# Kernel tuning notes

Hardware: AMD Instinct MI355X
Metric: run time of the kernel (lower is better)

The kernel has to match this reference:

```python
import jax, jax.numpy as jnp
import numpy as np

B, T, D = 4, 2048, 1024
H, Dh = 16, 64
Q_LAT, KV_LAT, O_LAT = 512, 256, 512
ROPE = 32
FFN_RANK, FFN_INTER = 384, 4096
EPS = 1e-6
THETA = 10000.0


def rms_norm(x, w, eps=EPS):
    xf = x.astype(jnp.float32)
    var = jnp.mean(xf * xf, axis=-1, keepdims=True)
    return (w * (xf * jax.lax.rsqrt(var + eps))).astype(x.dtype)


def rotate_half(x):
    x1, x2 = jnp.split(x, 2, axis=-1)
    return jnp.concatenate([-x2, x1], axis=-1)


def setup_inputs() -> dict:
    key = jax.random.key(0)
    ks = jax.random.split(key, 12)
    s = lambda fan_in: 1.0 / np.sqrt(fan_in)
    inp = {
        "hidden_states": jax.random.normal(ks[0], (B, T, D), jnp.float32),
        "ln1_w": jnp.ones((D,), jnp.float32),
        "a_ln_w": jnp.ones((Q_LAT + KV_LAT,), jnp.float32),
        "qkv_a_w": jax.random.normal(ks[1], (D, Q_LAT + KV_LAT), jnp.float32) * s(D),
        "q_b_w": jax.random.normal(ks[2], (Q_LAT, H * Dh), jnp.float32) * s(Q_LAT),
        "kv_b_w": jax.random.normal(ks[3], (KV_LAT, 2 * H * Dh), jnp.float32) * s(KV_LAT),
        "o_a_w": jax.random.normal(ks[4], (H * Dh, O_LAT), jnp.float32) * s(H * Dh),
        "o_b_w": jax.random.normal(ks[5], (O_LAT, D), jnp.float32) * s(O_LAT),
        "ln2_w": jnp.ones((D,), jnp.float32),
        "ffn_in_a": jax.random.normal(ks[6], (D, FFN_RANK), jnp.float32) * s(D),
        "ffn_in_b": jax.random.normal(ks[7], (FFN_RANK, FFN_INTER), jnp.float32) * s(FFN_RANK),
        "ffn_out_a": jax.random.normal(ks[8], (FFN_INTER, FFN_RANK), jnp.float32) * s(FFN_INTER),
        "ffn_out_b": jax.random.normal(ks[9], (FFN_RANK, D), jnp.float32) * s(FFN_RANK),
    }
    # RoPE tables over first ROPE dims of each head
    inv_freq = 1.0 / (THETA ** (np.arange(0, ROPE, 2, dtype=np.float32) / ROPE))
    t = np.arange(T, dtype=np.float32)
    freqs = np.outer(t, inv_freq)                      # [T, ROPE/2]
    emb = np.concatenate([freqs, freqs], axis=-1)      # [T, ROPE]
    inp["cos"] = jnp.asarray(np.cos(emb), jnp.float32)
    inp["sin"] = jnp.asarray(np.sin(emb), jnp.float32)
    return inp


def reference(hidden_states, cos, sin, ln1_w, a_ln_w, qkv_a_w, q_b_w, kv_b_w,
              o_a_w, o_b_w, ln2_w, ffn_in_a, ffn_in_b, ffn_out_a, ffn_out_b):
    x = hidden_states
    # --- MLA attention (pre-norm) ---
    h = rms_norm(x, ln1_w)
    lat = rms_norm(h @ qkv_a_w, a_ln_w)                # [B,T,Q_LAT+KV_LAT]
    q_lat, kv_lat = jnp.split(lat, [Q_LAT], axis=-1)
    q = (q_lat @ q_b_w).reshape(B, T, H, Dh).transpose(0, 2, 1, 3)   # [B,H,T,Dh]
    kv = (kv_lat @ kv_b_w).reshape(B, T, H, 2 * Dh).transpose(0, 2, 1, 3)
    k, v = jnp.split(kv, 2, axis=-1)
    # partial RoPE on first ROPE dims
    c = cos[None, None]; s_ = sin[None, None]          # [1,1,T,ROPE]
    q_r, q_p = q[..., :ROPE], q[..., ROPE:]
    k_r, k_p = k[..., :ROPE], k[..., ROPE:]
    q = jnp.concatenate([q_r * c + rotate_half(q_r) * s_, q_p], axis=-1)
    k = jnp.concatenate([k_r * c + rotate_half(k_r) * s_, k_p], axis=-1)
    scores = jnp.einsum("bhqd,bhkd->bhqk", q, k) * (Dh ** -0.5)
    attn = jax.nn.softmax(scores, axis=-1)
    ctx = jnp.einsum("bhqk,bhkd->bhqd", attn, v)
    ctx = ctx.transpose(0, 2, 1, 3).reshape(B, T, H * Dh)
    attn_out = (ctx @ o_a_w) @ o_b_w                   # output subspace
    x = x + attn_out
    # --- decomposed FFN (pre-norm) ---
    h2 = rms_norm(x, ln2_w)
    ff = jax.nn.gelu((h2 @ ffn_in_a) @ ffn_in_b)
    ff = (ff @ ffn_out_a) @ ffn_out_b
    return x + ff
```

## Files before the change

### kernel.cpp

```cpp
#include <hip/hip_runtime.h>
#include <hip/hip_bf16.h>
#include <stdint.h>

#define NTOK 8192

typedef unsigned short u16;
typedef __attribute__((ext_vector_type(4))) float f32x4;
typedef __attribute__((ext_vector_type(8))) short s16x8;
typedef __attribute__((ext_vector_type(4))) short s16x4;
typedef __attribute__((ext_vector_type(8))) u16   u16x8;
typedef __attribute__((ext_vector_type(4))) u16   u16x4;

__device__ __forceinline__ float fast_exp2(float x) {
    return __builtin_amdgcn_exp2f(x);
}
__device__ __forceinline__ u16 f2bf(float f) {
    uint32_t u = __float_as_uint(f);
    u = (u + 0x7FFFu + ((u >> 16) & 1u)) >> 16;
    return (u16)u;
}
__device__ __forceinline__ u16 f2bf_fast(float f) {
    return (u16)((__float_as_uint(f) + 0x8000u) >> 16);
}
__device__ __forceinline__ float bf2f(u16 h) {
    return __uint_as_float(((uint32_t)h) << 16);
}
__device__ __forceinline__ void async_cp16(const void* g, void* l) {
    __builtin_amdgcn_global_load_lds(
        (const __attribute__((address_space(1))) void*)g,
        (__attribute__((address_space(3))) void*)l, 16, 0, 0);
}
__device__ __forceinline__ void wait_vm4()   { asm volatile("s_waitcnt vmcnt(4)" ::: "memory"); }
__device__ __forceinline__ void wait_vm0()   { asm volatile("s_waitcnt vmcnt(0)" ::: "memory"); }
__device__ __forceinline__ void wait_lgkm0() { asm volatile("s_waitcnt lgkmcnt(0)" ::: "memory"); }
__device__ __forceinline__ void raw_barrier(){ asm volatile("s_barrier" ::: "memory"); }

struct TDesc { const float* s; u16* d; int K; int N; int tile0; };
struct TPack { TDesc t[8]; };

__global__ __launch_bounds__(256) void k_transpose_all(TPack p)
{
    __shared__ float tile[32][33];
    int bid = blockIdx.x;
    int i = 0;
    #pragma unroll
    for (int j = 1; j < 8; j++) if (bid >= p.t[j].tile0) i = j;
    const float* src = p.t[i].s;
    u16* dst = p.t[i].d;
    int K = p.t[i].K, N = p.t[i].N;
    int local = bid - p.t[i].tile0;
    int nx = N >> 5;
    int n0 = (local % nx) * 32, k0 = (local / nx) * 32;
    int tx = threadIdx.x, ty = threadIdx.y;
    #pragma unroll
    for (int r = 0; r < 32; r += 8)
        tile[ty + r][tx] = src[(size_t)(k0 + ty + r) * N + n0 + tx];
    __syncthreads();
    #pragma unroll
    for (int r = 0; r < 32; r += 8)
        dst[(size_t)(n0 + ty + r) * K + k0 + tx] = f2bf(tile[tx][ty + r]);
}

__global__ __launch_bounds__(256) void k_cvt(
    const float* __restrict__ in, u16* __restrict__ out)
{
    int i = (blockIdx.x * 256 + threadIdx.x) * 4;
    f32x4 v = *(const f32x4*)&in[i];
    u16x4 o;
    #pragma unroll
    for (int j = 0; j < 4; j++) o[j] = f2bf(v[j]);
    *(u16x4*)&out[i] = o;
}

template<int W>
__global__ __launch_bounds__(256) void k_rmsnorm(
    const float* __restrict__ x, const float* __restrict__ w, u16* __restrict__ out)
{
    constexpr int E = W / 256;
    int row = blockIdx.x, tid = threadIdx.x;
    const float* xr = x + (size_t)row * W;
    float v[E]; float ss = 0.f;
    #pragma unroll
    for (int i = 0; i < E; i++) { v[i] = xr[tid + i * 256]; ss += v[i] * v[i]; }
    #pragma unroll
    for (int m = 1; m < 64; m <<= 1) ss += __shfl_xor(ss, m, 64);
    __shared__ float red[4];
    if ((tid & 63) == 0) red[tid >> 6] = ss;
    __syncthreads();
    ss = red[0] + red[1] + red[2] + red[3];
    float scale = rsqrtf(ss / (float)W + 1e-6f);
    u16* orow = out + (size_t)row * W;
    #pragma unroll
    for (int i = 0; i < E; i++)
        orow[tid + i * 256] = f2bf(w[tid + i * 256] * (v[i] * scale));
}

template<int EPI>
__global__ __launch_bounds__(256) void k_gemm(
    const u16* __restrict__ A, int lda,
    const u16* __restrict__ Bt, int ldb,
    int M, int N, int K,
    float* __restrict__ outF, u16* __restrict__ outB,
    const float* __restrict__ resid)
{
    __shared__ __align__(16) u16 As[2][4096];
    __shared__ __align__(16) u16 Bs[2][4096];
    int tid = threadIdx.x;
    int w = tid >> 6, lane = tid & 63;
    int m0 = blockIdx.y * 128, n0 = blockIdx.x * 128;
    int wm = w & 1, wn = w >> 1;
    int lr = lane & 15, lq = lane >> 4;

    f32x4 acc[4][4];
    #pragma unroll
    for (int i = 0; i < 4; i++)
        #pragma unroll
        for (int j = 0; j < 4; j++) acc[i][j] = (f32x4)(0.f);

    int ar = tid >> 2;
    int ac = (tid & 3) * 8;
    const u16* Ag = A  + (size_t)(m0 + ar) * lda + ac;
    const u16* Bg = Bt + (size_t)(n0 + ar) * ldb + ac;
    int lo = w * 512;

    auto stage = [&](int kt, int s) {
        const u16* a  = Ag + kt * 32;
        const u16* bp = Bg + kt * 32;
        async_cp16(a,                     &As[s][lo]);
        async_cp16(a + (size_t)64 * lda,  &As[s][lo + 2048]);
        async_cp16(bp,                    &Bs[s][lo]);
        async_cp16(bp + (size_t)64 * ldb, &Bs[s][lo + 2048]);
    };

    int nk = K >> 5;
    stage(0, 0);
    stage(1, 1);
    for (int k = 0; k < nk; k++) {
        if (k + 1 < nk) wait_vm4(); else wait_vm0();
        raw_barrier();
        int s = k & 1;
        s16x8 af[4], bfr[4];
        #pragma unroll
        for (int ms = 0; ms < 4; ms++)
            af[ms] = *reinterpret_cast<const s16x8*>(&As[s][(wm * 64 + ms * 16 + lr) * 32 + lq * 8]);
        #pragma unroll
        for (int ns = 0; ns < 4; ns++)
            bfr[ns] = *reinterpret_cast<const s16x8*>(&Bs[s][(wn * 64 + ns * 16 + lr) * 32 + lq * 8]);
        #pragma unroll
        for (int ms = 0; ms < 4; ms++)
            #pragma unroll
            for (int ns = 0; ns < 4; ns++)
                acc[ms][ns] = __builtin_amdgcn_mfma_f32_16x16x32_bf16(af[ms], bfr[ns], acc[ms][ns], 0, 0, 0);
        wait_lgkm0();
        raw_barrier();
        if (k + 2 < nk) stage(k + 2, s);
    }

    #pragma unroll
    for (int ms = 0; ms < 4; ms++) {
        #pragma unroll
        for (int ns = 0; ns < 4; ns++) {
            int col = n0 + wn * 64 + ns * 16 + lr;
            #pragma unroll
            for (int r = 0; r < 4; r++) {
                int row = m0 + wm * 64 + ms * 16 + lq * 4 + r;
                float v = acc[ms][ns][r];
                size_t idx = (size_t)row * N + col;
                if (EPI == 0) {
                    outF[idx] = v;
                } else if (EPI == 1) {
                    outB[idx] = f2bf(v);
                } else if (EPI == 2) {
                    float t = 0.7978845608028654f * (v + 0.044715f * v * v * v);
                    outB[idx] = f2bf(0.5f * v * (1.f + tanhf(t)));
                } else {
                    outF[idx] = v + resid[idx];
                }
            }
        }
    }
}

template<int EPI>
__global__ __launch_bounds__(256) void k_gemm64(
    const u16* __restrict__ A, int lda,
    const u16* __restrict__ Bt, int ldb,
    int M, int N, int K,
    float* __restrict__ outF, u16* __restrict__ outB)
{
    __shared__ __align__(16) u16 As[2][4096];
    __shared__ __align__(16) u16 Bs[2][4096];
    int tid = threadIdx.x;
    int w = tid >> 6, lane = tid & 63;
    int m0 = blockIdx.y * 64, n0 = blockIdx.x * 64;
    int wm = w & 1, wn = w >> 1;
    int lr = lane & 15, lq = lane >> 4;

    f32x4 acc[2][2];
    #pragma unroll
    for (int i = 0; i < 2; i++)
        #pragma unroll
        for (int j = 0; j < 2; j++) acc[i][j] = (f32x4)(0.f);

    int srow = tid >> 2;
    int sq   = tid & 3;
    const u16* Ag = A  + (size_t)(m0 + srow) * lda + sq * 8;
    const u16* Bg = Bt + (size_t)(n0 + srow) * ldb + sq * 8;
    int lo = srow * 32 + sq * 8;

    auto stage = [&](int kt, int s) {
        const u16* a  = Ag + kt * 64;
        const u16* bp = Bg + kt * 64;
        async_cp16(a,       &As[s][lo]);
        async_cp16(a + 32,  &As[s][2048 + lo]);
        async_cp16(bp,      &Bs[s][lo]);
        async_cp16(bp + 32, &Bs[s][2048 + lo]);
    };

    int nk = K >> 6;
    stage(0, 0);
    stage(1, 1);
    for (int k = 0; k < nk; k++) {
        if (k + 1 < nk) wait_vm4(); else wait_vm0();
        raw_barrier();
        int s = k & 1;
        s16x8 af[2][2], bfr[2][2];
        #pragma unroll
        for (int kc = 0; kc < 2; kc++) {
            #pragma unroll
            for (int ms = 0; ms < 2; ms++)
                af[ms][kc] = *reinterpret_cast<const s16x8*>(
                    &As[s][kc * 2048 + (wm * 32 + ms * 16 + lr) * 32 + lq * 8]);
            #pragma unroll
            for (int ns = 0; ns < 2; ns++)
                bfr[ns][kc] = *reinterpret_cast<const s16x8*>(
                    &Bs[s][kc * 2048 + (wn * 32 + ns * 16 + lr) * 32 + lq * 8]);
        }
        #pragma unroll
        for (int kc = 0; kc < 2; kc++)
            #pragma unroll
            for (int ms = 0; ms < 2; ms++)
                #pragma unroll
                for (int ns = 0; ns < 2; ns++)
                    acc[ms][ns] = __builtin_amdgcn_mfma_f32_16x16x32_bf16(
                        af[ms][kc], bfr[ns][kc], acc[ms][ns], 0, 0, 0);
        wait_lgkm0();
        raw_barrier();
        if (k + 2 < nk) stage(k + 2, s);
    }

    #pragma unroll
    for (int ms = 0; ms < 2; ms++) {
        #pragma unroll
        for (int ns = 0; ns < 2; ns++) {
            int col = n0 + wn * 32 + ns * 16 + lr;
            #pragma unroll
            for (int r = 0; r < 4; r++) {
                int row = m0 + wm * 32 + ms * 16 + lq * 4 + r;
                float v = acc[ms][ns][r];
                size_t idx = (size_t)row * N + col;
                if (EPI == 0) outF[idx] = v;
                else          outB[idx] = f2bf(v);
            }
        }
    }
}

__global__ __launch_bounds__(256) void k_rope(
    const u16* __restrict__ q, const u16* __restrict__ kv,
    const float* __restrict__ cosb, const float* __restrict__ sinb,
    u16* __restrict__ q_r, u16* __restrict__ k_r)
{
    const float QS = 0.125f * 1.4426950408889634f;
    int idx = blockIdx.x * 256 + threadIdx.x;
    int g = idx & 7;
    int h = (idx >> 3) & 15;
    int t = (idx >> 7) & 2047;
    int b = idx >> 18;
    size_t qsrc = ((size_t)((b * 2048 + t) * 16 + h)) * 64 + g * 8;
    size_t ksrc = ((size_t)((b * 2048 + t) * 16 + h)) * 128 + g * 8;
    u16x8 qa = *(const u16x8*)&q[qsrc];
    u16x8 ka = *(const u16x8*)&kv[ksrc];
    u16x8 qo, ko;
    if (g < 4) {
        int pd = ((g ^ 2) - g) * 8;
        u16x8 qp = *(const u16x8*)&q[qsrc + pd];
        u16x8 kp = *(const u16x8*)&kv[ksrc + pd];
        float sgn = (g < 2) ? -1.f : 1.f;
        const float* cp = &cosb[t * 32 + g * 8];
        const float* sp = &sinb[t * 32 + g * 8];
        #pragma unroll
        for (int j = 0; j < 8; j++) {
            float c = cp[j], s = sp[j];
            qo[j] = f2bf((bf2f(qa[j]) * c + sgn * bf2f(qp[j]) * s) * QS);
            ko[j] = f2bf(bf2f(ka[j]) * c + sgn * bf2f(kp[j]) * s);
        }
    } else {
        #pragma unroll
        for (int j = 0; j < 8; j++) {
            qo[j] = f2bf(bf2f(qa[j]) * QS);
            ko[j] = ka[j];
        }
    }
    size_t dst = ((size_t)(b * 16 + h) * 2048 + t) * 64 + g * 8;
    *(u16x8*)&q_r[dst] = qo;
    *(u16x8*)&k_r[dst] = ko;
}

__global__ __launch_bounds__(256) void k_vtrans(
    const u16* __restrict__ kv, u16* __restrict__ v_t)
{
    __shared__ u16 tile[64][72];
    int bh = blockIdx.y;
    int b = bh >> 4, h = bh & 15;
    int t0 = blockIdx.x * 64;
    int tid = threadIdx.x;
    int r = tid >> 2;
    int c4 = (tid & 3) * 16;
    const u16* src = kv + ((size_t)((b * 2048 + t0 + r) * 16 + h)) * 128 + 64;
    #pragma unroll
    for (int j = 0; j < 16; j += 8)
        *(u16x8*)&tile[r][c4 + j] = *(const u16x8*)&src[c4 + j];
    __syncthreads();
    int dd = tid >> 2;
    u16* dst = v_t + ((size_t)bh * 64 + dd) * 2048 + t0;
    #pragma unroll
    for (int j0 = 0; j0 < 16; j0 += 8) {
        u16x8 vv;
        #pragma unroll
        for (int j = 0; j < 8; j++) vv[j] = tile[c4 + j0 + j][dd];
        *(u16x8*)&dst[c4 + j0] = vv;
    }
}

__global__ __launch_bounds__(256) void k_attn(
    const u16* __restrict__ q_r, const u16* __restrict__ k_r,
    const u16* __restrict__ v_t, u16* __restrict__ ctx)
{
    __shared__ __align__(16) u16 Ks[2][4096];
    __shared__ __align__(16) u16 Vs[2][4096];
    int tid = threadIdx.x, w = tid >> 6, lane = tid & 63;
    int bh = blockIdx.y;
    int b = bh >> 4, h = bh & 15;
    int q0 = blockIdx.x * 128 + w * 32;
    const u16* Qp = q_r + (size_t)bh * 2048 * 64;
    const u16* Kp = k_r + (size_t)bh * 2048 * 64;
    const u16* Vp = v_t + (size_t)bh * 64 * 2048;
    int lr = lane & 15, lq = lane >> 4;
    int swz = (lr >> 1) & 3;

    s16x8 qf[2][2];
    #pragma unroll
    for (int qc = 0; qc < 2; qc++)
        #pragma unroll
        for (int kf = 0; kf < 2; kf++)
            qf[qc][kf] = *(const s16x8*)&Qp[(size_t)(q0 + qc * 16 + lr) * 64 + kf * 32 + lq * 8];

    int schunk = ((lane & 3) ^ ((lane >> 3) & 3)) * 8;
    const u16* gstage;
    u16 *lp0, *lp1;
    size_t grow;
    if (w < 2) {
        gstage = Kp + (size_t)(lane >> 2) * 64 + w * 32 + schunk;
        lp0 = &Ks[0][w * 2048]; lp1 = &Ks[1][w * 2048];
        grow = 16 * 64;
    } else {
        gstage = Vp + (size_t)(lane >> 2) * 2048 + (w - 2) * 32 + schunk;
        lp0 = &Vs[0][(w - 2) * 2048]; lp1 = &Vs[1][(w - 2) * 2048];
        grow = 16 * 2048;
    }
    auto stage = [&](int kt, int s) {
        size_t goff = (w < 2) ? (size_t)kt * 64 : (size_t)kt;
        u16* lp = s ? lp1 : lp0;
        #pragma unroll
        for (int g = 0; g < 4; g++)
            async_cp16(gstage + goff + g * grow, lp + g * 512);
    };

    float l0 = 0.f, l1 = 0.f;
    f32x4 o[2][4];
    #pragma unroll
    for (int qt = 0; qt < 2; qt++)
        #pragma unroll
        for (int ds = 0; ds < 4; ds++) o[qt][ds] = (f32x4)(0.f);

    stage(0, 0);
    stage(64, 1);
    for (int k = 0; k < 32; k++) {
        if (k < 31) wait_vm4(); else wait_vm0();
        raw_barrier();
        int s = k & 1;
        const u16* Ksb = Ks[s];
        const u16* Vsb = Vs[s];

        f32x4 sc[2][4];
        #pragma unroll
        for (int ns = 0; ns < 4; ns++) {
            int ko = (ns * 16 + lr) * 32 + ((lq ^ swz) * 8);
            s16x8 a0 = *(const s16x8*)&Ksb[ko];
            s16x8 a1 = *(const s16x8*)&Ksb[2048 + ko];
            #pragma unroll
            for (int qc = 0; qc < 2; qc++) {
                f32x4 t = (f32x4)(0.f);
                t = __builtin_amdgcn_mfma_f32_16x16x32_bf16(a0, qf[qc][0], t, 0, 0, 0);
                t = __builtin_amdgcn_mfma_f32_16x16x32_bf16(a1, qf[qc][1], t, 0, 0, 0);
                sc[qc][ns] = t;
            }
        }

        float rs0 = 0.f, rs1 = 0.f;
        #pragma unroll
        for (int kf = 0; kf < 2; kf++) {
            s16x8 pk0, pk1;
            #pragma unroll
            for (int hh = 0; hh < 2; hh++) {
                int ns = kf * 2 + hh;
                #pragma unroll
                for (int r = 0; r < 4; r++) {
                    float p0 = fast_exp2(sc[0][ns][r]);
                    float p1 = fast_exp2(sc[1][ns][r]);
                    rs0 += p0; rs1 += p1;
                    pk0[hh * 4 + r] = (short)f2bf_fast(p0);
                    pk1[hh * 4 + r] = (short)f2bf_fast(p1);
                }
            }
            #pragma unroll
            for (int ds = 0; ds < 4; ds++) {
                int vbase = kf * 2048 + (ds * 16 + lr) * 32 + (lq & 1) * 4;
                s16x4 vlo = *(const s16x4*)&Vsb[vbase + (((lq >> 1)    ) ^ swz) * 8];
                s16x4 vhi = *(const s16x4*)&Vsb[vbase + (((lq >> 1) | 2) ^ swz) * 8];
                s16x8 vf = __builtin_shufflevector(vlo, vhi, 0, 1, 2, 3, 4, 5, 6, 7);
                o[0][ds] = __builtin_amdgcn_mfma_f32_16x16x32_bf16(pk0, vf, o[0][ds], 0, 0, 0);
                o[1][ds] = __builtin_amdgcn_mfma_f32_16x16x32_bf16(pk1, vf, o[1][ds], 0, 0, 0);
            }
        }
        rs0 += __shfl_xor(rs0, 16, 64);
        rs0 += __shfl_xor(rs0, 32, 64);
        rs1 += __shfl_xor(rs1, 16, 64);
        rs1 += __shfl_xor(rs1, 32, 64);
        l0 += rs0;
        l1 += rs1;

        wait_lgkm0();
        raw_barrier();
        if (k + 2 < 32) stage((k + 2) * 64, s);
    }

    #pragma unroll
    for (int qt = 0; qt < 2; qt++) {
        float lv = qt ? l1 : l0;
        float li[4];
        #pragma unroll
        for (int r = 0; r < 4; r++) li[r] = 1.f / __shfl(lv, lq * 4 + r, 64);
        #pragma unroll
        for (int ds = 0; ds < 4; ds++)
            #pragma unroll
            for (int r = 0; r < 4; r++) {
                int tq = q0 + qt * 16 + lq * 4 + r;
                float v = o[qt][ds][r] * li[r];
                ctx[((size_t)(b * 2048) + tq) * 1024 + h * 64 + ds * 16 + lr] = f2bf(v);
            }
    }
}

extern "C" void kernel_launch(void* const* d_in, const int* in_sizes, int n_in,
                              void* d_out, int out_size, void* d_ws, size_t ws_size,
                              hipStream_t stream) {
    (void)in_sizes; (void)n_in; (void)out_size; (void)ws_size;
    const float* x     = (const float*)d_in[0];
    const float* ln1   = (const float*)d_in[1];
    const float* alnw  = (const float*)d_in[2];
    const float* qkv_a = (const float*)d_in[3];
    const float* q_b   = (const float*)d_in[4];
    const float* kv_b  = (const float*)d_in[5];
    const float* o_a   = (const float*)d_in[6];
    const float* o_b   = (const float*)d_in[7];
    const float* ln2   = (const float*)d_in[8];
    const float* in_a  = (const float*)d_in[9];
    const float* in_b  = (const float*)d_in[10];
    const float* out_a = (const float*)d_in[11];
    const float* out_b = (const float*)d_in[12];
    const float* cosb  = (const float*)d_in[13];
    const float* sinb  = (const float*)d_in[14];
    float* out = (float*)d_out;
    char* ws = (char*)d_ws;

    u16* wqkv = (u16*)ws;
    u16* wq   = wqkv + 786432;
    u16* wkv  = wq   + 524288;
    u16* wob  = wkv  + 524288;
    u16* wia  = wob  + 524288;
    u16* wib  = wia  + 393216;
    u16* woa2 = wib  + 1572864;
    u16* wob2 = woa2 + 1572864;
    u16* woan = wob2 + 393216;
    u16* woab = woan + 524288;

    char* G = ws + 15728640;
    u16*  hbuf  = (u16*)(G + 0);
    float* lat_raw = (float*)(G + 16777216);
    u16*  lat   = (u16*)(G + 41943040);
    u16*  qbuf  = (u16*)(G + 54525952);
    u16*  kvbuf = (u16*)(G + 71303168);
    u16*  q_r   = (u16*)(G + 0);
    u16*  k_r   = (u16*)(G + 16777216);
    u16*  v_t   = (u16*)(G + 33554432);
    u16*  ctx   = (u16*)(G + 54525952);
    float* x2   = (float*)(G + 0);
    u16*  h2    = (u16*)(G + 33554432);
    u16*  t1    = (u16*)(G + 50331648);
    u16*  t2    = (u16*)(G + 56623104);
    u16*  t3    = (u16*)(G + 50331648);

    TPack tp;
    tp.t[0] = { qkv_a, wqkv, 1024, 768,  0 };
    tp.t[1] = { q_b,   wq,   512,  1024, 768 };
    tp.t[2] = { kv_b,  wkv,  256,  2048, 1280 };
    tp.t[3] = { o_b,   wob,  512,  1024, 1792 };
    tp.t[4] = { in_a,  wia,  1024, 384,  2304 };
    tp.t[5] = { in_b,  wib,  384,  4096, 2688 };
    tp.t[6] = { out_a, woa2, 4096, 384,  4224 };
    tp.t[7] = { out_b, wob2, 384,  1024, 5760 };
    k_transpose_all<<<6144, dim3(32, 8), 0, stream>>>(tp);
    k_cvt<<<512, 256, 0, stream>>>(o_a, woan);
    k_gemm64<1><<<dim3(16, 16), 256, 0, stream>>>(wob, 512, woan, 512, 1024, 1024, 512, nullptr, woab);

    k_rmsnorm<1024><<<NTOK, 256, 0, stream>>>(x, ln1, hbuf);
    k_gemm64<0><<<dim3(12, 128), 256, 0, stream>>>(hbuf, 1024, wqkv, 1024, NTOK, 768, 1024, lat_raw, nullptr);
    k_rmsnorm<768><<<NTOK, 256, 0, stream>>>(lat_raw, alnw, lat);
    k_gemm<1><<<dim3(8, 64),  256, 0, stream>>>(lat,       768, wq,  512, NTOK, 1024, 512, nullptr, qbuf,  nullptr);
    k_gemm<1><<<dim3(16, 64), 256, 0, stream>>>(lat + 512, 768, wkv, 256, NTOK, 2048, 256, nullptr, kvbuf, nullptr);
    k_rope<<<4096, 256, 0, stream>>>(qbuf, kvbuf, cosb, sinb, q_r, k_r);
    k_vtrans<<<dim3(32, 64), 256, 0, stream>>>(kvbuf, v_t);
    k_attn<<<dim3(16, 64), 256, 0, stream>>>(q_r, k_r, v_t, ctx);
    k_gemm<3><<<dim3(8, 64), 256, 0, stream>>>(ctx, 1024, woab, 1024, NTOK, 1024, 1024, x2, nullptr, x);
    k_rmsnorm<1024><<<NTOK, 256, 0, stream>>>(x2, ln2, h2);
    k_gemm64<1><<<dim3(6, 128), 256, 0, stream>>>(h2, 1024, wia, 1024, NTOK, 384, 1024, nullptr, t1);
    k_gemm<2><<<dim3(32, 64), 256, 0, stream>>>(t1, 384, wib, 384, NTOK, 4096, 384, nullptr, t2, nullptr);
    k_gemm64<1><<<dim3(6, 128), 256, 0, stream>>>(t2, 4096, woa2, 4096, NTOK, 384, 4096, nullptr, t3);
    k_gemm<3><<<dim3(8, 64), 256, 0, stream>>>(t3, 384, wob2, 384, NTOK, 1024, 384, out, nullptr, x2);
}
```

Measured before the change: 539.3 us.

## Compute softmax row sums via MFMA, packed bf16 convert, unroll double-buffer loop

The attention kernel now gets the softmax denominators from an extra MFMA of the probability tile against a ones vector. This replaces the scalar adds and cross-lane shuffles per iteration. Probabilities are converted with the hardware v_cvt_pk_bf16_f32 instruction instead of manual rounding. The K/V double-buffer loop is unrolled by two with constant buffer indices and incremented global pointers, and s_setprio is raised around the MFMA sections. The row sums are now taken from bf16-rounded probabilities, which slightly changes numerics, and each tile costs two extra MFMAs.

```diff
diff --git a/kernel.cpp b/kernel.cpp
--- a/kernel.cpp
+++ b/kernel.cpp
@@ -10,6 +10,7 @@
 typedef __attribute__((ext_vector_type(4))) short s16x4;
 typedef __attribute__((ext_vector_type(8))) u16   u16x8;
 typedef __attribute__((ext_vector_type(4))) u16   u16x4;
+typedef __attribute__((ext_vector_type(4))) uint32_t u32x4;
 
 __device__ __forceinline__ float fast_exp2(float x) {
     return __builtin_amdgcn_exp2f(x);
@@ -18,9 +19,6 @@
     uint32_t u = __float_as_uint(f);
     u = (u + 0x7FFFu + ((u >> 16) & 1u)) >> 16;
     return (u16)u;
-}
-__device__ __forceinline__ u16 f2bf_fast(float f) {
-    return (u16)((__float_as_uint(f) + 0x8000u) >> 16);
 }
 __device__ __forceinline__ float bf2f(u16 h) {
     return __uint_as_float(((uint32_t)h) << 16);
@@ -356,102 +354,114 @@
         for (int kf = 0; kf < 2; kf++)
             qf[qc][kf] = *(const s16x8*)&Qp[(size_t)(q0 + qc * 16 + lr) * 64 + kf * 32 + lq * 8];
 
+    s16x8 ones;
+    #pragma unroll
+    for (int j = 0; j < 8; j++) ones[j] = (short)0x3F80;
+
     int schunk = ((lane & 3) ^ ((lane >> 3) & 3)) * 8;
-    const u16* gstage;
+    const u16* gp;
     u16 *lp0, *lp1;
     size_t grow;
+    int gAdv;
     if (w < 2) {
-        gstage = Kp + (size_t)(lane >> 2) * 64 + w * 32 + schunk;
+        gp = Kp + (size_t)(lane >> 2) * 64 + w * 32 + schunk;
         lp0 = &Ks[0][w * 2048]; lp1 = &Ks[1][w * 2048];
-        grow = 16 * 64;
+        grow = 16 * 64;  gAdv = 64 * 64;
     } else {
-        gstage = Vp + (size_t)(lane >> 2) * 2048 + (w - 2) * 32 + schunk;
+        gp = Vp + (size_t)(lane >> 2) * 2048 + (w - 2) * 32 + schunk;
         lp0 = &Vs[0][(w - 2) * 2048]; lp1 = &Vs[1][(w - 2) * 2048];
-        grow = 16 * 2048;
-    }
-    auto stage = [&](int kt, int s) {
-        size_t goff = (w < 2) ? (size_t)kt * 64 : (size_t)kt;
-        u16* lp = s ? lp1 : lp0;
+        grow = 16 * 2048; gAdv = 64;
+    }
+    auto stageP = [&](u16* lp) {
         #pragma unroll
         for (int g = 0; g < 4; g++)
-            async_cp16(gstage + goff + g * grow, lp + g * 512);
+            async_cp16(gp + g * grow, lp + g * 512);
+        gp += gAdv;
     };
 
-    float l0 = 0.f, l1 = 0.f;
     f32x4 o[2][4];
     #pragma unroll
     for (int qt = 0; qt < 2; qt++)
         #pragma unroll
         for (int ds = 0; ds < 4; ds++) o[qt][ds] = (f32x4)(0.f);
-
-    stage(0, 0);
-    stage(64, 1);
-    for (int k = 0; k < 32; k++) {
-        if (k < 31) wait_vm4(); else wait_vm0();
-        raw_barrier();
-        int s = k & 1;
-        const u16* Ksb = Ks[s];
-        const u16* Vsb = Vs[s];
-
-        f32x4 sc[2][4];
-        #pragma unroll
-        for (int ns = 0; ns < 4; ns++) {
-            int ko = (ns * 16 + lr) * 32 + ((lq ^ swz) * 8);
-            s16x8 a0 = *(const s16x8*)&Ksb[ko];
-            s16x8 a1 = *(const s16x8*)&Ksb[2048 + ko];
-            #pragma unroll
-            for (int qc = 0; qc < 2; qc++) {
-                f32x4 t = (f32x4)(0.f);
-                t = __builtin_amdgcn_mfma_f32_16x16x32_bf16(a0, qf[qc][0], t, 0, 0, 0);
-                t = __builtin_amdgcn_mfma_f32_16x16x32_bf16(a1, qf[qc][1], t, 0, 0, 0);
-                sc[qc][ns] = t;
-            }
-        }
-
-        float rs0 = 0.f, rs1 = 0.f;
-        #pragma unroll
-        for (int kf = 0; kf < 2; kf++) {
-            s16x8 pk0, pk1;
-            #pragma unroll
-            for (int hh = 0; hh < 2; hh++) {
-                int ns = kf * 2 + hh;
-                #pragma unroll
-                for (int r = 0; r < 4; r++) {
-                    float p0 = fast_exp2(sc[0][ns][r]);
-                    float p1 = fast_exp2(sc[1][ns][r]);
-                    rs0 += p0; rs1 += p1;
-                    pk0[hh * 4 + r] = (short)f2bf_fast(p0);
-                    pk1[hh * 4 + r] = (short)f2bf_fast(p1);
-                }
-            }
-            #pragma unroll
-            for (int ds = 0; ds < 4; ds++) {
-                int vbase = kf * 2048 + (ds * 16 + lr) * 32 + (lq & 1) * 4;
-                s16x4 vlo = *(const s16x4*)&Vsb[vbase + (((lq >> 1)    ) ^ swz) * 8];
-                s16x4 vhi = *(const s16x4*)&Vsb[vbase + (((lq >> 1) | 2) ^ swz) * 8];
-                s16x8 vf = __builtin_shufflevector(vlo, vhi, 0, 1, 2, 3, 4, 5, 6, 7);
-                o[0][ds] = __builtin_amdgcn_mfma_f32_16x16x32_bf16(pk0, vf, o[0][ds], 0, 0, 0);
-                o[1][ds] = __builtin_amdgcn_mfma_f32_16x16x32_bf16(pk1, vf, o[1][ds], 0, 0, 0);
-            }
-        }
-        rs0 += __shfl_xor(rs0, 16, 64);
-        rs0 += __shfl_xor(rs0, 32, 64);
-        rs1 += __shfl_xor(rs1, 16, 64);
-        rs1 += __shfl_xor(rs1, 32, 64);
-        l0 += rs0;
-        l1 += rs1;
-
-        wait_lgkm0();
-        raw_barrier();
-        if (k + 2 < 32) stage((k + 2) * 64, s);
-    }
+    f32x4 lacc0 = (f32x4)(0.f), lacc1 = (f32x4)(0.f);
+
+#define ATTN_BODY(S)                                                           \
+  {                                                                            \
+    f32x4 sc[2][4];                                                            \
+    __builtin_amdgcn_s_setprio(1);                                             \
+    _Pragma("unroll")                                                          \
+    for (int ns = 0; ns < 4; ns++) {                                           \
+      int ko = (ns * 16 + lr) * 32 + ((lq ^ swz) * 8);                         \
+      s16x8 a0 = *(const s16x8*)&Ks[S][ko];                                    \
+      s16x8 a1 = *(const s16x8*)&Ks[S][2048 + ko];                             \
+      _Pragma("unroll")                                                        \
+      for (int qc = 0; qc < 2; qc++) {                                         \
+        f32x4 t = (f32x4)(0.f);                                                \
+        t = __builtin_amdgcn_mfma_f32_16x16x32_bf16(a0, qf[qc][0], t, 0, 0, 0);\
+        t = __builtin_amdgcn_mfma_f32_16x16x32_bf16(a1, qf[qc][1], t, 0, 0, 0);\
+        sc[qc][ns] = t;                                                        \
+      }                                                                        \
+    }                                                                          \
+    __builtin_amdgcn_s_setprio(0);                                             \
+    _Pragma("unroll")                                                          \
+    for (int kf = 0; kf < 2; kf++) {                                           \
+      u32x4 w0, w1;                                                            \
+      _Pragma("unroll")                                                        \
+      for (int j = 0; j < 4; j++) {                                            \
+        int ns = kf * 2 + (j >> 1);                                            \
+        int r0 = (j & 1) * 2;                                                  \
+        float ea = fast_exp2(sc[0][ns][r0]);                                   \
+        float eb = fast_exp2(sc[0][ns][r0 + 1]);                               \
+        float ec = fast_exp2(sc[1][ns][r0]);                                   \
+        float ed = fast_exp2(sc[1][ns][r0 + 1]);                               \
+        uint32_t t0, t1;                                                       \
+        asm("v_cvt_pk_bf16_f32 %0, %1, %2" : "=v"(t0) : "v"(ea), "v"(eb));     \
+        asm("v_cvt_pk_bf16_f32 %0, %1, %2" : "=v"(t1) : "v"(ec), "v"(ed));     \
+        w0[j] = t0; w1[j] = t1;                                                \
+      }                                                                        \
+      s16x8 pk0 = __builtin_bit_cast(s16x8, w0);                               \
+      s16x8 pk1 = __builtin_bit_cast(s16x8, w1);                               \
+      __builtin_amdgcn_s_setprio(1);                                           \
+      lacc0 = __builtin_amdgcn_mfma_f32_16x16x32_bf16(pk0, ones, lacc0, 0,0,0);\
+      lacc1 = __builtin_amdgcn_mfma_f32_16x16x32_bf16(pk1, ones, lacc1, 0,0,0);\
+      _Pragma("unroll")                                                        \
+      for (int ds = 0; ds < 4; ds++) {                                         \
+        int vbase = kf * 2048 + (ds * 16 + lr) * 32 + (lq & 1) * 4;            \
+        s16x4 vlo = *(const s16x4*)&Vs[S][vbase + (((lq >> 1)    ) ^ swz) * 8];\
+        s16x4 vhi = *(const s16x4*)&Vs[S][vbase + (((lq >> 1) | 2) ^ swz) * 8];\
+        s16x8 vf = __builtin_shufflevector(vlo, vhi, 0, 1, 2, 3, 4, 5, 6, 7);  \
+        o[0][ds] = __builtin_amdgcn_mfma_f32_16x16x32_bf16(pk0, vf, o[0][ds], 0, 0, 0);\
+        o[1][ds] = __builtin_amdgcn_mfma_f32_16x16x32_bf16(pk1, vf, o[1][ds], 0, 0, 0);\
+      }                                                                        \
+      __builtin_amdgcn_s_setprio(0);                                           \
+    }                                                                          \
+  }
+
+    stageP(lp0);
+    stageP(lp1);
+    for (int k2 = 0; k2 < 15; k2++) {
+        wait_vm4(); raw_barrier();
+        ATTN_BODY(0)
+        wait_lgkm0(); raw_barrier();
+        stageP(lp0);
+        wait_vm4(); raw_barrier();
+        ATTN_BODY(1)
+        wait_lgkm0(); raw_barrier();
+        stageP(lp1);
+    }
+    wait_vm4(); raw_barrier();
+    ATTN_BODY(0)
+    wait_vm0(); raw_barrier();
+    ATTN_BODY(1)
+#undef ATTN_BODY
 
     #pragma unroll
     for (int qt = 0; qt < 2; qt++) {
-        float lv = qt ? l1 : l0;
+        f32x4 lv = qt ? lacc1 : lacc0;
         float li[4];
         #pragma unroll
-        for (int r = 0; r < 4; r++) li[r] = 1.f / __shfl(lv, lq * 4 + r, 64);
+        for (int r = 0; r < 4; r++) li[r] = 1.f / lv[r];
         #pragma unroll
         for (int ds = 0; ds < 4; ds++)
             #pragma unroll
```

Measured after the change: 523.0 us. 3.0% less time.
